# Optimization experiments

Hardware: AMD Instinct MI355X
Metric: run time of the kernel (lower is better)

Reference implementation:

```python
import jax, jax.numpy as jnp
import numpy as np

B, L, H, Q = 64, 512, 1024, 64
VA_H = 256


def setup_inputs() -> dict:
    key = jax.random.key(0)
    ks = jax.random.split(key, 10)
    hidden_states = jax.random.normal(ks[0], (B, L, H), dtype=jnp.float32)
    quad_spans = jax.random.randint(ks[1], (B, Q, 4), 0, L, dtype=jnp.int64)
    quad_mask = jnp.ones((B, Q), dtype=jnp.int32)
    s = 0.02
    W1 = jax.random.normal(ks[2], (3 * H, VA_H), dtype=jnp.float32) * s
    b1 = jnp.zeros((VA_H,), dtype=jnp.float32)
    W2 = jax.random.normal(ks[3], (VA_H, VA_H // 2), dtype=jnp.float32) * s
    b2 = jnp.zeros((VA_H // 2,), dtype=jnp.float32)
    W3 = jax.random.normal(ks[4], (VA_H // 2, 2), dtype=jnp.float32) * s
    b3 = jnp.zeros((2,), dtype=jnp.float32)
    return {"hidden_states": hidden_states, "quad_spans": quad_spans,
            "quad_mask": quad_mask, "W1": W1, "b1": b1, "W2": W2, "b2": b2,
            "W3": W3, "b3": b3}


def _pool_spans(hidden_states, quad_spans, quad_mask):
    # hidden_states [B,L,H]; quad_spans [B,Q,4]; quad_mask [B,Q]
    Bn, Ln, Hn = hidden_states.shape
    pos = jnp.arange(Ln)[None, None, :]                      # [1,1,L]
    asp_s = quad_spans[:, :, 0:1]
    asp_e = quad_spans[:, :, 1:2]
    opi_s = quad_spans[:, :, 2:3]
    opi_e = quad_spans[:, :, 3:4]
    asp_valid = asp_s >= 2
    opi_valid = opi_s >= 2
    sep = pos == 1                                           # [SEP] fallback
    asp_m = ((pos >= asp_s) & (pos <= asp_e) & asp_valid) | (~asp_valid & sep)
    opi_m = ((pos >= opi_s) & (pos <= opi_e) & opi_valid) | (~opi_valid & sep)
    qm = (quad_mask != 0)[:, :, None]
    asp_f = (asp_m & qm).astype(hidden_states.dtype)         # [B,Q,L]
    opi_f = (opi_m & qm).astype(hidden_states.dtype)
    h_asp = jnp.einsum('bql,blh->bqh', asp_f, hidden_states) / jnp.clip(
        asp_f.sum(-1, keepdims=True), 1.0, None)
    h_opi = jnp.einsum('bql,blh->bqh', opi_f, hidden_states) / jnp.clip(
        opi_f.sum(-1, keepdims=True), 1.0, None)
    return h_asp, h_opi


def reference(hidden_states, quad_spans, quad_mask, W1, b1, W2, b2, W3, b3):
    h_asp, h_opi = _pool_spans(hidden_states, quad_spans, quad_mask)
    h_pair = jnp.concatenate([h_asp, h_opi, h_asp * h_opi], axis=-1)  # [B,Q,3H]
    x = jax.nn.gelu(h_pair @ W1 + b1, approximate=False)   # torch GELU = exact
    x = jax.nn.gelu(x @ W2 + b2, approximate=False)        # dropout: eval mode
    x = x @ W3 + b3                                        # [B,Q,2]
    va = jax.nn.sigmoid(x) * 8.0 + 1.0
    return va * quad_mask[:, :, None].astype(va.dtype)
```

## Files before the change

### kernel.cpp

```cpp
#include <hip/hip_runtime.h>
#include <math.h>


typedef __attribute__((ext_vector_type(4))) float f32x4;
typedef __attribute__((ext_vector_type(8))) short bf16x8;

#define NPAIR 4096
#define LSEQ 512
#define HDIM 1024

#if defined(__has_builtin)
#if __has_builtin(__builtin_amdgcn_global_load_lds)
#define HAVE_GLDS 1
#endif
#endif
#ifndef HAVE_GLDS
#define HAVE_GLDS 0
#endif

__device__ __forceinline__ unsigned int pack2(float lo, float hi) {
  const unsigned int a = __float_as_uint(lo) + 0x8000u;
  const unsigned int b = __float_as_uint(hi) + 0x8000u;
  return __builtin_amdgcn_perm(b, a, 0x07060302u);
}
__device__ __forceinline__ unsigned short f2bf(float f) {
  return (unsigned short)((__float_as_uint(f) + 0x8000u) >> 16);
}
__device__ __forceinline__ float gelu(float x) {
  return 0.5f * x * (1.f + erff(x * 0.70710678118654752f));
}

__global__ __launch_bounds__(256, 4) void pool_mfma_kernel(
    const float* __restrict__ hs, const int* __restrict__ spans,
    const int* __restrict__ qmask, unsigned short* __restrict__ hpair) {
  __shared__ __align__(16) unsigned char smem[34816];
  __shared__ float scl[128];
  typedef unsigned short BlT[64][40];
  BlT* Bl = (BlT*)smem;
  float(*S)[68] = (float(*)[68])smem;

  const int b = blockIdx.x >> 4;
  const int n0 = (blockIdx.x & 15) * 64;
  const int tid = threadIdx.x;
  const int lane = tid & 63;
  const int lm = lane & 15, quad = lane >> 4;
  const int wm = (tid >> 6) * 32;

  const bool is64 =
      (spans[1] == 0) && (spans[3] == 0) && (spans[5] == 0) && (spans[7] == 0);

  auto span_of = [&](int r, int& s, int& e) {
    const int q = r & 63, t = r >> 6;
    const int idx = (b * 64 + q) * 4 + t * 2;
    s = is64 ? spans[idx * 2] : spans[idx];
    e = is64 ? spans[idx * 2 + 2] : spans[idx + 1];
    if (s < 2) { s = 1; e = 1; }
  };
  int s0, e0, s1, e1;
  span_of(wm + lm, s0, e0);
  span_of(wm + 16 + lm, s1, e1);

  if (tid < 128) {
    int s, e;
    span_of(tid, s, e);
    const int c = (e >= s) ? (e - s + 1) : 0;
    const float sc = 1.f / (float)(c < 1 ? 1 : c);
    scl[tid] = (qmask[b * 64 + (tid & 63)] != 0) ? sc : 0.f;
  }

  f32x4 acc[2][4];
#pragma unroll
  for (int f = 0; f < 2; ++f)
#pragma unroll
    for (int g = 0; g < 4; ++g) acc[f][g] = f32x4{0.f, 0.f, 0.f, 0.f};

  const float* hsb = hs + (size_t)b * (LSEQ * HDIM);
  const int nl = tid & 63;
  const int kw = (tid >> 6) * 8;

  auto load8 = [&](int kbase, unsigned int (&tmp)[4]) {
    const float* src = hsb + (size_t)(kbase + kw) * HDIM + n0 + nl;
#pragma unroll
    for (int i = 0; i < 4; ++i) {
      const float f0 = src[(size_t)(2 * i) * HDIM];
      const float f1 = src[(size_t)(2 * i + 1) * HDIM];
      tmp[i] = pack2(f0, f1);
    }
  };

  unsigned int tmp[4];
  load8(0, tmp);
  *(uint4*)&Bl[0][nl][kw] = make_uint4(tmp[0], tmp[1], tmp[2], tmp[3]);

  for (int it = 0; it < 16; ++it) {
    const int k0 = it * 32;
    __syncthreads();
    if (it < 15) load8(k0 + 32, tmp);

    bf16x8 a0, a1;
#pragma unroll
    for (int j = 0; j < 8; ++j) {
      const int k = k0 + quad * 8 + j;
      a0[j] = (short)((k >= s0 && k <= e0) ? 0x3F80 : 0);
      a1[j] = (short)((k >= s1 && k <= e1) ? 0x3F80 : 0);
    }
    const BlT& Bc = Bl[it & 1];
#pragma unroll
    for (int g = 0; g < 4; ++g) {
      bf16x8 bg = *(const bf16x8*)&Bc[g * 16 + lm][quad * 8];
      acc[0][g] = __builtin_amdgcn_mfma_f32_16x16x32_bf16(a0, bg, acc[0][g], 0, 0, 0);
      acc[1][g] = __builtin_amdgcn_mfma_f32_16x16x32_bf16(a1, bg, acc[1][g], 0, 0, 0);
    }
    if (it < 15) {
      *(uint4*)&Bl[(it + 1) & 1][nl][kw] = make_uint4(tmp[0], tmp[1], tmp[2], tmp[3]);
    }
  }

  __syncthreads();
#pragma unroll
  for (int f = 0; f < 2; ++f)
#pragma unroll
    for (int g = 0; g < 4; ++g)
#pragma unroll
      for (int r = 0; r < 4; ++r)
        S[wm + f * 16 + quad * 4 + r][g * 16 + lm] = acc[f][g][r];
  __syncthreads();

  const int q = tid >> 2;
  const int cg = (tid & 3) * 16;
  const float sA = scl[q], sO = scl[64 + q];
  unsigned short* dst = hpair + (size_t)(b * 64 + q) * 3072 + n0 + cg;
#pragma unroll
  for (int h = 0; h < 2; ++h) {
    float a[8], o[8];
#pragma unroll
    for (int i = 0; i < 8; ++i) {
      a[i] = S[q][cg + h * 8 + i] * sA;
      o[i] = S[64 + q][cg + h * 8 + i] * sO;
    }
    uint4 wa, wo, wp;
    wa.x = pack2(a[0], a[1]); wa.y = pack2(a[2], a[3]);
    wa.z = pack2(a[4], a[5]); wa.w = pack2(a[6], a[7]);
    wo.x = pack2(o[0], o[1]); wo.y = pack2(o[2], o[3]);
    wo.z = pack2(o[4], o[5]); wo.w = pack2(o[6], o[7]);
    wp.x = pack2(a[0] * o[0], a[1] * o[1]); wp.y = pack2(a[2] * o[2], a[3] * o[3]);
    wp.z = pack2(a[4] * o[4], a[5] * o[5]); wp.w = pack2(a[6] * o[6], a[7] * o[7]);
    *(uint4*)(dst + h * 8) = wa;
    *(uint4*)(dst + 1024 + h * 8) = wo;
    *(uint4*)(dst + 2048 + h * 8) = wp;
  }
}

__global__ void transpose_two(const float* __restrict__ W1,
                              unsigned short* __restrict__ W1T,
                              const float* __restrict__ W2,
                              unsigned short* __restrict__ W2T) {
  __shared__ float t[32][33];
  const float* in;
  unsigned short* out;
  int R, C, c0, r0;
  int blk = blockIdx.x;
  if (blk < 768) {
    in = W1; out = W1T; R = 3072; C = 256;
    c0 = (blk & 7) * 32; r0 = (blk >> 3) * 32;
  } else {
    blk -= 768;
    in = W2; out = W2T; R = 256; C = 128;
    c0 = (blk & 3) * 32; r0 = (blk >> 2) * 32;
  }
  const int x = threadIdx.x, y = threadIdx.y;
#pragma unroll
  for (int i = 0; i < 32; i += 8)
    t[y + i][x] = in[(size_t)(r0 + y + i) * C + c0 + x];
  __syncthreads();
#pragma unroll
  for (int i = 0; i < 32; i += 8)
    out[(size_t)(c0 + y + i) * R + r0 + x] = f2bf(t[x][y + i]);
}

__global__ __launch_bounds__(256) void gemm_bt_128(
    const unsigned short* __restrict__ A, const unsigned short* __restrict__ Bt,
    float* __restrict__ P, int M, int N, int K, int KH) {
  __shared__ __align__(16) unsigned short Al[2][128][32];
  __shared__ __align__(16) unsigned short Bl[2][128][32];
  const int bm = blockIdx.x * 128, bn = blockIdx.y * 128;
  const int kz = blockIdx.z * KH;
  const int tid = threadIdx.x;
  const int wave = tid >> 6, lane = tid & 63;
  const int wm = (wave & 1) * 64, wn = (wave >> 1) * 64;
  const int lm = lane & 15, lk = (lane >> 4) * 8;

  const int srow = wave * 32 + (lane >> 2);
  const int scol = (lane & 3) * 8;
  const unsigned short* ga = A + (size_t)(bm + srow) * K + kz + scol;
  const unsigned short* gb = Bt + (size_t)(bn + srow) * K + kz + scol;
  unsigned short* laA[2] = {&Al[0][wave * 32][0], &Al[1][wave * 32][0]};
  unsigned short* laB[2] = {&Bl[0][wave * 32][0], &Bl[1][wave * 32][0]};

  f32x4 acc[4][4];
#pragma unroll
  for (int i = 0; i < 4; ++i)
#pragma unroll
    for (int j = 0; j < 4; ++j) acc[i][j] = f32x4{0.f, 0.f, 0.f, 0.f};

  auto stage = [&](int u, int k0) {
#if HAVE_GLDS
    __builtin_amdgcn_global_load_lds(ga + k0, laA[u], 16, 0, 0);
    __builtin_amdgcn_global_load_lds(ga + (size_t)16 * K + k0, laA[u] + 16 * 32, 16, 0, 0);
    __builtin_amdgcn_global_load_lds(gb + k0, laB[u], 16, 0, 0);
    __builtin_amdgcn_global_load_lds(gb + (size_t)16 * K + k0, laB[u] + 16 * 32, 16, 0, 0);
#else
    *(uint4*)(laA[u] + lane * 8) = *(const uint4*)(ga + k0);
    *(uint4*)(laA[u] + 16 * 32 + lane * 8) = *(const uint4*)(ga + (size_t)16 * K + k0);
    *(uint4*)(laB[u] + lane * 8) = *(const uint4*)(gb + k0);
    *(uint4*)(laB[u] + 16 * 32 + lane * 8) = *(const uint4*)(gb + (size_t)16 * K + k0);
#endif
  };

  const int NT = KH / 32;
  stage(0, 0);
  for (int t = 0; t < NT; ++t) {
    __syncthreads();
    if (t + 1 < NT) stage((t + 1) & 1, (t + 1) * 32);
    const int u = t & 1;
    bf16x8 af[4], bf[4];
#pragma unroll
    for (int i = 0; i < 4; ++i) {
      af[i] = *(const bf16x8*)&Al[u][wm + i * 16 + lm][lk];
      bf[i] = *(const bf16x8*)&Bl[u][wn + i * 16 + lm][lk];
    }
#pragma unroll
    for (int i = 0; i < 4; ++i)
#pragma unroll
      for (int j = 0; j < 4; ++j)
        acc[i][j] = __builtin_amdgcn_mfma_f32_16x16x32_bf16(af[i], bf[j], acc[i][j], 0, 0, 0);
  }

  float* Pz = P + (size_t)blockIdx.z * M * N;
  const int rq = (lane >> 4) << 2;
#pragma unroll
  for (int i = 0; i < 4; ++i)
#pragma unroll
    for (int j = 0; j < 4; ++j) {
      const int r0 = bm + wm + i * 16 + rq;
      const int c0 = bn + wn + j * 16 + lm;
#pragma unroll
      for (int r = 0; r < 4; ++r)
        Pz[(size_t)(r0 + r) * N + c0] = acc[i][j][r];
    }
}

__global__ __launch_bounds__(256) void tail_kernel(
    const float* __restrict__ P, const float* __restrict__ b1,
    const unsigned short* __restrict__ W2T, const float* __restrict__ b2,
    const float* __restrict__ W3, const float* __restrict__ b3,
    const int* __restrict__ qmask, float* __restrict__ out) {
  __shared__ __align__(16) unsigned short Al[16 * 264];
  __shared__ float S2[16][132];
  __shared__ float w3[256];

  const int m0 = blockIdx.x * 16;
  const int tid = threadIdx.x;
  const int wave = tid >> 6, lane = tid & 63;
  const int lm = lane & 15, quad = lane >> 4;
  const int wn = wave * 32;

  w3[tid] = W3[tid];

  {
    const int row = tid >> 4;
    const int slot = tid & 15;
#pragma unroll
    for (int ss = 0; ss < 2; ++ss) {
      const int s = slot + ss * 16;
      const float* pb = P + (size_t)(m0 + row) * 256 + s * 8;
      float v[8];
      {
        float4 ba = *(const float4*)(b1 + s * 8);
        float4 bb = *(const float4*)(b1 + s * 8 + 4);
        v[0] = ba.x; v[1] = ba.y; v[2] = ba.z; v[3] = ba.w;
        v[4] = bb.x; v[5] = bb.y; v[6] = bb.z; v[7] = bb.w;
      }
#pragma unroll
      for (int z = 0; z < 4; ++z) {
        const float* pz = pb + (size_t)z * ((size_t)NPAIR * 256);
        float4 a0 = *(const float4*)pz;
        float4 a1 = *(const float4*)(pz + 4);
        v[0] += a0.x; v[1] += a0.y; v[2] += a0.z; v[3] += a0.w;
        v[4] += a1.x; v[5] += a1.y; v[6] += a1.z; v[7] += a1.w;
      }
      uint4 w;
      w.x = pack2(gelu(v[0]), gelu(v[1]));
      w.y = pack2(gelu(v[2]), gelu(v[3]));
      w.z = pack2(gelu(v[4]), gelu(v[5]));
      w.w = pack2(gelu(v[6]), gelu(v[7]));
      *(uint4*)((char*)Al + (size_t)row * 528 + s * 16) = w;
    }
  }
  __syncthreads();

  f32x4 acc[2];
  acc[0] = f32x4{0.f, 0.f, 0.f, 0.f};
  acc[1] = f32x4{0.f, 0.f, 0.f, 0.f};
#pragma unroll
  for (int ks = 0; ks < 8; ++ks) {
    bf16x8 a = *(const bf16x8*)((char*)Al + (size_t)lm * 528 + ks * 64 + quad * 16);
#pragma unroll
    for (int g = 0; g < 2; ++g) {
      const int n = wn + g * 16 + lm;
      bf16x8 b = *(const bf16x8*)(W2T + (size_t)n * 256 + ks * 32 + quad * 8);
      acc[g] = __builtin_amdgcn_mfma_f32_16x16x32_bf16(a, b, acc[g], 0, 0, 0);
    }
  }

#pragma unroll
  for (int g = 0; g < 2; ++g) {
    const int col = wn + g * 16 + lm;
    const float bc = b2[col];
#pragma unroll
    for (int r = 0; r < 4; ++r) S2[quad * 4 + r][col] = gelu(acc[g][r] + bc);
  }
  __syncthreads();

  if (tid < 128) {
    const int row = tid >> 3, o = (tid >> 2) & 1, q4 = tid & 3;
    float part = 0.f;
#pragma unroll 8
    for (int c = q4; c < 128; c += 4) part += S2[row][c] * w3[c * 2 + o];
    part += __shfl_xor(part, 1);
    part += __shfl_xor(part, 2);
    if (q4 == 0) {
      const int pair = m0 + row;
      const float a = part + b3[o];
      const float qmf = (float)qmask[pair];
      out[pair * 2 + o] = ((1.f / (1.f + expf(-a))) * 8.f + 1.f) * qmf;
    }
  }
}

extern "C" void kernel_launch(void* const* d_in, const int* in_sizes, int n_in,
                              void* d_out, int out_size, void* d_ws,
                              size_t ws_size, hipStream_t stream) {
  const float* hs = (const float*)d_in[0];
  const int* spans = (const int*)d_in[1];
  const int* qmask = (const int*)d_in[2];
  const float* W1 = (const float*)d_in[3];
  const float* b1 = (const float*)d_in[4];
  const float* W2 = (const float*)d_in[5];
  const float* b2 = (const float*)d_in[6];
  const float* W3 = (const float*)d_in[7];
  const float* b3 = (const float*)d_in[8];
  float* out = (float*)d_out;

  const size_t HPAIR_B = 25165824;
  const size_t P_B = 16777216;
  const size_t W1T_B = 1572864;

  char* ws = (char*)d_ws;
  size_t off = 0;
  unsigned short* hpair = (unsigned short*)(ws + off); off += HPAIR_B;
  float* P = (float*)(ws + off);                       off += P_B;
  unsigned short* W1T = (unsigned short*)(ws + off);   off += W1T_B;
  unsigned short* W2T = (unsigned short*)(ws + off);

  transpose_two<<<800, dim3(32, 8), 0, stream>>>(W1, W1T, W2, W2T);
  pool_mfma_kernel<<<1024, 256, 0, stream>>>(hs, spans, qmask, hpair);
  gemm_bt_128<<<dim3(32, 2, 4), 256, 0, stream>>>(hpair, W1T, P, NPAIR,
                                                  256, 3072, 768);
  tail_kernel<<<256, 256, 0, stream>>>(P, b1, W2T, b2, W3, b3, qmask, out);
}
```

Before: 237.2 us.

## Merge weight transpose into pooling launch and retile GEMM to 64x256

```diff
diff --git a/kernel.cpp b/kernel.cpp
--- a/kernel.cpp
+++ b/kernel.cpp
@@ -30,18 +30,46 @@
   return 0.5f * x * (1.f + erff(x * 0.70710678118654752f));
 }
 
-__global__ __launch_bounds__(256, 4) void pool_mfma_kernel(
+__global__ __launch_bounds__(256, 4) void prep_kernel(
     const float* __restrict__ hs, const int* __restrict__ spans,
-    const int* __restrict__ qmask, unsigned short* __restrict__ hpair) {
+    const int* __restrict__ qmask, unsigned short* __restrict__ hpair,
+    const float* __restrict__ W1, unsigned short* __restrict__ W1T,
+    const float* __restrict__ W2, unsigned short* __restrict__ W2T) {
   __shared__ __align__(16) unsigned char smem[34816];
   __shared__ float scl[128];
+  const int tid = threadIdx.x;
+
+  if (blockIdx.x >= 1024) {
+    float(*t)[33] = (float(*)[33])smem;
+    const float* in;
+    unsigned short* out;
+    int C, R, c0, r0;
+    int blk = blockIdx.x - 1024;
+    if (blk < 768) {
+      in = W1; out = W1T; R = 3072; C = 256;
+      c0 = (blk & 7) * 32; r0 = (blk >> 3) * 32;
+    } else {
+      blk -= 768;
+      in = W2; out = W2T; R = 256; C = 128;
+      c0 = (blk & 3) * 32; r0 = (blk >> 2) * 32;
+    }
+    const int x = tid & 31, y = tid >> 5;
+#pragma unroll
+    for (int i = 0; i < 32; i += 8)
+      t[y + i][x] = in[(size_t)(r0 + y + i) * C + c0 + x];
+    __syncthreads();
+#pragma unroll
+    for (int i = 0; i < 32; i += 8)
+      out[(size_t)(c0 + y + i) * R + r0 + x] = f2bf(t[x][y + i]);
+    return;
+  }
+
   typedef unsigned short BlT[64][40];
   BlT* Bl = (BlT*)smem;
   float(*S)[68] = (float(*)[68])smem;
 
   const int b = blockIdx.x >> 4;
   const int n0 = (blockIdx.x & 15) * 64;
-  const int tid = threadIdx.x;
   const int lane = tid & 63;
   const int lm = lane & 15, quad = lane >> 4;
   const int wm = (tid >> 6) * 32;
@@ -151,51 +179,22 @@
   }
 }
 
-__global__ void transpose_two(const float* __restrict__ W1,
-                              unsigned short* __restrict__ W1T,
-                              const float* __restrict__ W2,
-                              unsigned short* __restrict__ W2T) {
-  __shared__ float t[32][33];
-  const float* in;
-  unsigned short* out;
-  int R, C, c0, r0;
-  int blk = blockIdx.x;
-  if (blk < 768) {
-    in = W1; out = W1T; R = 3072; C = 256;
-    c0 = (blk & 7) * 32; r0 = (blk >> 3) * 32;
-  } else {
-    blk -= 768;
-    in = W2; out = W2T; R = 256; C = 128;
-    c0 = (blk & 3) * 32; r0 = (blk >> 2) * 32;
-  }
-  const int x = threadIdx.x, y = threadIdx.y;
-#pragma unroll
-  for (int i = 0; i < 32; i += 8)
-    t[y + i][x] = in[(size_t)(r0 + y + i) * C + c0 + x];
-  __syncthreads();
-#pragma unroll
-  for (int i = 0; i < 32; i += 8)
-    out[(size_t)(c0 + y + i) * R + r0 + x] = f2bf(t[x][y + i]);
-}
-
-__global__ __launch_bounds__(256) void gemm_bt_128(
+__global__ __launch_bounds__(256) void gemm_bt_64x256(
     const unsigned short* __restrict__ A, const unsigned short* __restrict__ Bt,
     float* __restrict__ P, int M, int N, int K, int KH) {
-  __shared__ __align__(16) unsigned short Al[2][128][32];
-  __shared__ __align__(16) unsigned short Bl[2][128][32];
-  const int bm = blockIdx.x * 128, bn = blockIdx.y * 128;
+  __shared__ __align__(16) unsigned short Al[2][64][32];
+  __shared__ __align__(16) unsigned short Bl[2][256][32];
+  const int bm = blockIdx.x * 64;
   const int kz = blockIdx.z * KH;
   const int tid = threadIdx.x;
   const int wave = tid >> 6, lane = tid & 63;
-  const int wm = (wave & 1) * 64, wn = (wave >> 1) * 64;
+  const int wn = wave * 64;
   const int lm = lane & 15, lk = (lane >> 4) * 8;
 
-  const int srow = wave * 32 + (lane >> 2);
+  const int srow = lane >> 2;
   const int scol = (lane & 3) * 8;
-  const unsigned short* ga = A + (size_t)(bm + srow) * K + kz + scol;
-  const unsigned short* gb = Bt + (size_t)(bn + srow) * K + kz + scol;
-  unsigned short* laA[2] = {&Al[0][wave * 32][0], &Al[1][wave * 32][0]};
-  unsigned short* laB[2] = {&Bl[0][wave * 32][0], &Bl[1][wave * 32][0]};
+  const unsigned short* ga = A + (size_t)(bm + wave * 16 + srow) * K + kz + scol;
+  const unsigned short* gb = Bt + (size_t)(wn + srow) * K + kz + scol;
 
   f32x4 acc[4][4];
 #pragma unroll
@@ -205,15 +204,17 @@
 
   auto stage = [&](int u, int k0) {
 #if HAVE_GLDS
-    __builtin_amdgcn_global_load_lds(ga + k0, laA[u], 16, 0, 0);
-    __builtin_amdgcn_global_load_lds(ga + (size_t)16 * K + k0, laA[u] + 16 * 32, 16, 0, 0);
-    __builtin_amdgcn_global_load_lds(gb + k0, laB[u], 16, 0, 0);
-    __builtin_amdgcn_global_load_lds(gb + (size_t)16 * K + k0, laB[u] + 16 * 32, 16, 0, 0);
+    __builtin_amdgcn_global_load_lds(ga + k0, &Al[u][wave * 16][0], 16, 0, 0);
+#pragma unroll
+    for (int c = 0; c < 4; ++c)
+      __builtin_amdgcn_global_load_lds(gb + (size_t)(c * 16) * K + k0,
+                                       &Bl[u][wn + c * 16][0], 16, 0, 0);
 #else
-    *(uint4*)(laA[u] + lane * 8) = *(const uint4*)(ga + k0);
-    *(uint4*)(laA[u] + 16 * 32 + lane * 8) = *(const uint4*)(ga + (size_t)16 * K + k0);
-    *(uint4*)(laB[u] + lane * 8) = *(const uint4*)(gb + k0);
-    *(uint4*)(laB[u] + 16 * 32 + lane * 8) = *(const uint4*)(gb + (size_t)16 * K + k0);
+    *(uint4*)&Al[u][wave * 16 + srow][scol] = *(const uint4*)(ga + k0);
+#pragma unroll
+    for (int c = 0; c < 4; ++c)
+      *(uint4*)&Bl[u][wn + c * 16 + srow][scol] =
+          *(const uint4*)(gb + (size_t)(c * 16) * K + k0);
 #endif
   };
 
@@ -226,7 +227,7 @@
     bf16x8 af[4], bf[4];
 #pragma unroll
     for (int i = 0; i < 4; ++i) {
-      af[i] = *(const bf16x8*)&Al[u][wm + i * 16 + lm][lk];
+      af[i] = *(const bf16x8*)&Al[u][i * 16 + lm][lk];
       bf[i] = *(const bf16x8*)&Bl[u][wn + i * 16 + lm][lk];
     }
 #pragma unroll
@@ -242,8 +243,8 @@
   for (int i = 0; i < 4; ++i)
 #pragma unroll
     for (int j = 0; j < 4; ++j) {
-      const int r0 = bm + wm + i * 16 + rq;
-      const int c0 = bn + wn + j * 16 + lm;
+      const int r0 = bm + i * 16 + rq;
+      const int c0 = wn + j * 16 + lm;
 #pragma unroll
       for (int r = 0; r < 4; ++r)
         Pz[(size_t)(r0 + r) * N + c0] = acc[i][j][r];
@@ -363,9 +364,8 @@
   unsigned short* W1T = (unsigned short*)(ws + off);   off += W1T_B;
   unsigned short* W2T = (unsigned short*)(ws + off);
 
-  transpose_two<<<800, dim3(32, 8), 0, stream>>>(W1, W1T, W2, W2T);
-  pool_mfma_kernel<<<1024, 256, 0, stream>>>(hs, spans, qmask, hpair);
-  gemm_bt_128<<<dim3(32, 2, 4), 256, 0, stream>>>(hpair, W1T, P, NPAIR,
-                                                  256, 3072, 768);
+  prep_kernel<<<1824, 256, 0, stream>>>(hs, spans, qmask, hpair, W1, W1T, W2, W2T);
+  gemm_bt_64x256<<<dim3(64, 1, 4), 256, 0, stream>>>(hpair, W1T, P, NPAIR,
+                                                     256, 3072, 768);
   tail_kernel<<<256, 256, 0, stream>>>(P, b1, W2T, b2, W3, b3, qmask, out);
 }
```

Result: no change. 238.9 us (+0.7%).
